# Kernel tuning notes

Measured on AMD Instinct MI355X. Metric: run time of the kernel, lower is better.

The kernel has to match this reference:

```python
import jax, jax.numpy as jnp
import numpy as np

N_NODES = 100000
N_EDGES = 1600000
IN_C, HID_C, OUT_C = 128, 128, 64


def setup_inputs() -> dict:
    key = jax.random.key(0)
    ks = jax.random.split(key, 6)
    x = jax.random.normal(ks[0], (N_NODES, IN_C), dtype=jnp.float32)
    edge_index = jax.random.randint(ks[1], (2, N_EDGES), 0, N_NODES)
    W1 = jax.random.normal(ks[2], (IN_C, HID_C), dtype=jnp.float32) * (1.0 / np.sqrt(IN_C))
    b1 = jnp.zeros((HID_C,), dtype=jnp.float32)
    W2 = jax.random.normal(ks[3], (HID_C, OUT_C), dtype=jnp.float32) * (1.0 / np.sqrt(HID_C))
    b2 = jnp.zeros((OUT_C,), dtype=jnp.float32)
    return {"x": x, "edge_index": edge_index, "W1": W1, "b1": b1, "W2": W2, "b2": b2}


def gcn_conv(x, W, b, src, dst):
    # PyG GCNConv: D^{-1/2} (A + I) D^{-1/2} X W + b, with self-loops handled
    # analytically (no explicit self-loop edges materialized).
    h = x @ W                                             # [N, d_out]
    ones = jnp.ones(src.shape[0], dtype=h.dtype)
    deg = jax.ops.segment_sum(ones, dst, num_segments=N_NODES) + 1.0  # +1 self-loop
    dinv = jax.lax.rsqrt(deg)                             # deg >= 1, safe
    norm = dinv[src] * dinv[dst]                          # [E]
    msg = h[src] * norm[:, None]                          # gather + scale  [E, d_out]
    agg = jax.ops.segment_sum(msg, dst, num_segments=N_NODES)
    agg = agg + h * (dinv * dinv)[:, None]                # self-loop contribution
    return agg + b


def reference(x, edge_index, W1, b1, W2, b2):
    src, dst = edge_index[0], edge_index[1]
    h = jax.nn.relu(gcn_conv(x, W1, b1, src, dst))
    # dropout is identity in eval mode
    out = gcn_conv(h, W2, b2, src, dst)
    return out
```

## Files before the change

### kernel.cpp

```cpp
#include <hip/hip_runtime.h>

#define N_NODESC 100000
#define N_EDGESC 1600000
#define NB_BUCKETS 391
#define BUCKET_CAP 5120
#define CHUNK_A 4096

typedef __attribute__((ext_vector_type(4))) float floatx4;
typedef __attribute__((ext_vector_type(8))) short shortx8;

__device__ __forceinline__ unsigned short f32_to_bf16_rne(float f) {
    unsigned int u = __float_as_uint(f);
    unsigned int r = u + 0x7fffu + ((u >> 16) & 1u);
    return (unsigned short)(r >> 16);
}
__device__ __forceinline__ float bf16_to_f32(unsigned short h) {
    return __uint_as_float(((unsigned int)h) << 16);
}
__device__ __forceinline__ float bflo(unsigned int u) { return __uint_as_float(u << 16); }
__device__ __forceinline__ float bfhi(unsigned int u) { return __uint_as_float(u & 0xffff0000u); }
__device__ __forceinline__ unsigned int pack2bf(float a, float b) {
    return ((unsigned int)f32_to_bf16_rne(b) << 16) | (unsigned int)f32_to_bf16_rne(a);
}

__global__ __launch_bounds__(256) void k_wfrag_all(const float* __restrict__ W1,
        const float* __restrict__ W2,
        unsigned short* __restrict__ w1hi, unsigned short* __restrict__ w1lo,
        unsigned short* __restrict__ w2hi, unsigned short* __restrict__ w2lo,
        int* __restrict__ gcur) {
    int t = threadIdx.x;
    if (blockIdx.x == 0)
        for (int i = t; i < NB_BUCKETS; i += 256) gcur[i] = i * BUCKET_CAP;
    int idx = blockIdx.x * 256 + t;
    float f;
    int k, col, C, o;
    unsigned short *phi, *plo;
    if (idx < 16384) {
        k = idx >> 7; col = idx & 127; C = 8;
        f = W1[idx]; phi = w1hi; plo = w1lo;
    } else {
        int idx2 = idx - 16384;
        k = idx2 >> 6; col = idx2 & 63; C = 4;
        f = W2[idx2]; phi = w2hi; plo = w2lo;
    }
    unsigned short hi = f32_to_bf16_rne(f);
    unsigned short lo = f32_to_bf16_rne(f - bf16_to_f32(hi));
    int kc = k >> 5, q = (k >> 3) & 3, j = k & 7;
    int c = col >> 4, n = col & 15;
    o = (((kc * C + c) * 4 + q) * 16 + n) * 8 + j;
    phi[o] = hi; plo[o] = lo;
}

__global__ __launch_bounds__(1024) void k_bucket(const int* __restrict__ src,
        const int* __restrict__ dst, int* __restrict__ gcur,
        unsigned int* __restrict__ tmp) {
    __shared__ int hist[NB_BUCKETS];
    int t = threadIdx.x;
    for (int i = t; i < NB_BUCKETS; i += 1024) hist[i] = 0;
    __syncthreads();
    int base = blockIdx.x * CHUNK_A;
    int end = min(base + CHUNK_A, N_EDGESC);
    for (int e = base + t; e < end; e += 1024)
        atomicAdd(&hist[dst[e] >> 8], 1);
    __syncthreads();
    for (int i = t; i < NB_BUCKETS; i += 1024) {
        int c = hist[i];
        hist[i] = (c > 0) ? atomicAdd(&gcur[i], c) : 0;
    }
    __syncthreads();
    for (int e = base + t; e < end; e += 1024) {
        int d = dst[e];
        int pos = atomicAdd(&hist[d >> 8], 1);
        tmp[pos] = ((unsigned int)src[e] << 8) | (unsigned int)(d & 255);
    }
}

__global__ __launch_bounds__(1024) void k_place(const unsigned int* __restrict__ tmp,
        const int* __restrict__ gcur,
        int* __restrict__ swsrc, int* __restrict__ deg,
        int* __restrict__ row_ptr, float* __restrict__ dinv) {
    __shared__ int hist[256], scan[256], lcur[256];
    int b = blockIdx.x, t = threadIdx.x;
    int start = b * BUCKET_CAP;
    int end = gcur[b];
    if (t < 256) hist[t] = 0;
    __syncthreads();
    for (int i = start + t; i < end; i += 1024)
        atomicAdd(&hist[tmp[i] & 255u], 1);
    __syncthreads();
    int own = (t < 256) ? hist[t] : 0;
    if (t < 256) scan[t] = own;
    __syncthreads();
    for (int off = 1; off < 256; off <<= 1) {
        int add = (t >= off && t < 256) ? scan[t - off] : 0;
        __syncthreads();
        if (t < 256) scan[t] += add;
        __syncthreads();
    }
    if (t < 256) {
        int rp = start + scan[t] - own;
        lcur[t] = rp;
        int node = (b << 8) + t;
        if (node < N_NODESC) {
            deg[node] = own;
            row_ptr[node] = rp;
            dinv[node] = rsqrtf((float)own + 1.0f);
        }
    }
    __syncthreads();
    for (int i = start + t; i < end; i += 1024) {
        unsigned int v = tmp[i];
        int pos = atomicAdd(&lcur[v & 255u], 1);
        swsrc[pos] = (int)(v >> 8);
    }
}

template<int NOUT, int AFP32>
__global__ __launch_bounds__(256) void k_gemm_mfma(const void* __restrict__ Xv,
        const unsigned short* __restrict__ whi, const unsigned short* __restrict__ wlo,
        const float* __restrict__ dinv, unsigned short* __restrict__ H) {
    constexpr int C = NOUT / 16;
    constexpr int PITCH = NOUT + 4;
    __shared__ __align__(16) float etile[4][16][PITCH];
    int wv = threadIdx.x >> 6, lane = threadIdx.x & 63;
    int n16 = lane & 15, q = lane >> 4;
    int rowBase = blockIdx.x * 128 + wv * 32;
    floatx4 acc[2][C];
#pragma unroll
    for (int m = 0; m < 2; ++m)
#pragma unroll
        for (int c = 0; c < C; ++c) acc[m][c] = (floatx4){0.f, 0.f, 0.f, 0.f};

    const shortx8* whi8 = (const shortx8*)whi;
    const shortx8* wlo8 = (const shortx8*)wlo;

    for (int kc = 0; kc < 4; ++kc) {
        shortx8 ahi[2], alo[2];
#pragma unroll
        for (int m = 0; m < 2; ++m) {
            int r = rowBase + m * 16 + n16;
            if (r >= N_NODESC) r = N_NODESC - 1;
            if (AFP32) {
                const float* xp = &((const float*)Xv)[(size_t)r * 128 + kc * 32 + q * 8];
                floatx4 x0 = *(const floatx4*)xp;
                floatx4 x1 = *(const floatx4*)(xp + 4);
#pragma unroll
                for (int jj = 0; jj < 4; ++jj) {
                    unsigned short h0 = f32_to_bf16_rne(x0[jj]);
                    ahi[m][jj] = (short)h0;
                    alo[m][jj] = (short)f32_to_bf16_rne(x0[jj] - bf16_to_f32(h0));
                    unsigned short h1 = f32_to_bf16_rne(x1[jj]);
                    ahi[m][jj + 4] = (short)h1;
                    alo[m][jj + 4] = (short)f32_to_bf16_rne(x1[jj] - bf16_to_f32(h1));
                }
            } else {
                const unsigned short* xp = &((const unsigned short*)Xv)[(size_t)r * 128 + kc * 32 + q * 8];
                ahi[m] = *(const shortx8*)xp;
            }
        }
#pragma unroll
        for (int c = 0; c < C; ++c) {
            int fo = (kc * C + c) * 64 + lane;
            shortx8 bhi = whi8[fo];
            shortx8 blo = wlo8[fo];
#pragma unroll
            for (int m = 0; m < 2; ++m) {
                acc[m][c] = __builtin_amdgcn_mfma_f32_16x16x32_bf16(ahi[m], bhi, acc[m][c], 0, 0, 0);
                if (AFP32)
                    acc[m][c] = __builtin_amdgcn_mfma_f32_16x16x32_bf16(alo[m], bhi, acc[m][c], 0, 0, 0);
                acc[m][c] = __builtin_amdgcn_mfma_f32_16x16x32_bf16(ahi[m], blo, acc[m][c], 0, 0, 0);
            }
        }
    }
    constexpr int CPL = NOUT / 4;
#pragma unroll
    for (int m = 0; m < 2; ++m) {
        __builtin_amdgcn_wave_barrier();
#pragma unroll
        for (int c = 0; c < C; ++c)
#pragma unroll
            for (int reg = 0; reg < 4; ++reg)
                etile[wv][q * 4 + reg][c * 16 + n16] = acc[m][c][reg];
        asm volatile("s_waitcnt lgkmcnt(0)" ::: "memory");
        __builtin_amdgcn_wave_barrier();
        int row = lane >> 2, cb = lane & 3;
        int r = rowBase + m * 16 + row;
        if (r < N_NODESC) {
            float dv = dinv[r];
            unsigned int po[CPL / 2];
#pragma unroll
            for (int i = 0; i < CPL / 4; ++i) {
                floatx4 v = *(const floatx4*)&etile[wv][row][cb * CPL + i * 4];
                po[i * 2 + 0] = pack2bf(v[0] * dv, v[1] * dv);
                po[i * 2 + 1] = pack2bf(v[2] * dv, v[3] * dv);
            }
            unsigned int* op = (unsigned int*)&H[(size_t)r * NOUT + cb * CPL];
#pragma unroll
            for (int i = 0; i < CPL / 8; ++i)
                *(uint4*)(op + i * 4) = *(uint4*)&po[i * 4];
        }
        asm volatile("s_waitcnt lgkmcnt(0)" ::: "memory");
        __builtin_amdgcn_wave_barrier();
    }
}

__global__ __launch_bounds__(256) void k_agg_gemm(const unsigned short* __restrict__ Hb,
        const int* __restrict__ swsrc, const int* __restrict__ row_ptr,
        const int* __restrict__ deg, const float* __restrict__ dinv,
        const float* __restrict__ bias,
        const unsigned short* __restrict__ w2hi, const unsigned short* __restrict__ w2lo,
        unsigned short* __restrict__ H2) {
    __shared__ __align__(16) unsigned int lds_h[16][64];
    int wv = threadIdx.x >> 6, lane = threadIdx.x & 63;
    int g = lane >> 4, l16 = lane & 15;
    int nb = blockIdx.x * 16;

#pragma unroll
    for (int i = 0; i < 4; ++i) {
        int nt = wv * 4 + i;
        int node = nb + nt;
        int start = row_ptr[node];
        int end = start + deg[node];
        float acc[8] = {0.f, 0.f, 0.f, 0.f, 0.f, 0.f, 0.f, 0.f};
        int j = start + g;
        for (; j + 4 < end; j += 8) {
            int s0 = swsrc[j];
            int s1 = swsrc[j + 4];
            uint4 v0 = *(const uint4*)(Hb + (size_t)s0 * 128 + l16 * 8);
            uint4 v1 = *(const uint4*)(Hb + (size_t)s1 * 128 + l16 * 8);
            acc[0] += bflo(v0.x) + bflo(v1.x);
            acc[1] += bfhi(v0.x) + bfhi(v1.x);
            acc[2] += bflo(v0.y) + bflo(v1.y);
            acc[3] += bfhi(v0.y) + bfhi(v1.y);
            acc[4] += bflo(v0.z) + bflo(v1.z);
            acc[5] += bfhi(v0.z) + bfhi(v1.z);
            acc[6] += bflo(v0.w) + bflo(v1.w);
            acc[7] += bfhi(v0.w) + bfhi(v1.w);
        }
        if (j < end) {
            int s0 = swsrc[j];
            uint4 v0 = *(const uint4*)(Hb + (size_t)s0 * 128 + l16 * 8);
            acc[0] += bflo(v0.x); acc[1] += bfhi(v0.x);
            acc[2] += bflo(v0.y); acc[3] += bfhi(v0.y);
            acc[4] += bflo(v0.z); acc[5] += bfhi(v0.z);
            acc[6] += bflo(v0.w); acc[7] += bfhi(v0.w);
        }
#pragma unroll
        for (int k = 0; k < 8; ++k) {
            acc[k] += __shfl_xor(acc[k], 16);
            acc[k] += __shfl_xor(acc[k], 32);
        }
        if (g == 0) {
            float dv = dinv[node];
            uint4 sv = *(const uint4*)(Hb + (size_t)node * 128 + l16 * 8);
            floatx4 b0 = *(const floatx4*)&bias[l16 * 8];
            floatx4 b1 = *(const floatx4*)&bias[l16 * 8 + 4];
            float o0 = dv * (acc[0] + bflo(sv.x)) + b0[0];
            float o1 = dv * (acc[1] + bfhi(sv.x)) + b0[1];
            float o2 = dv * (acc[2] + bflo(sv.y)) + b0[2];
            float o3 = dv * (acc[3] + bfhi(sv.y)) + b0[3];
            float o4 = dv * (acc[4] + bflo(sv.z)) + b1[0];
            float o5 = dv * (acc[5] + bfhi(sv.z)) + b1[1];
            float o6 = dv * (acc[6] + bflo(sv.w)) + b1[2];
            float o7 = dv * (acc[7] + bfhi(sv.w)) + b1[3];
            uint4 o;
            o.x = pack2bf(fmaxf(o0, 0.f), fmaxf(o1, 0.f));
            o.y = pack2bf(fmaxf(o2, 0.f), fmaxf(o3, 0.f));
            o.z = pack2bf(fmaxf(o4, 0.f), fmaxf(o5, 0.f));
            o.w = pack2bf(fmaxf(o6, 0.f), fmaxf(o7, 0.f));
            int pcol = (l16 * 4) ^ ((nt & 7) * 4);
            *(uint4*)&lds_h[nt][pcol] = o;
        }
    }
    __syncthreads();

    int q = lane >> 4, n16 = lane & 15;
    floatx4 accm = (floatx4){0.f, 0.f, 0.f, 0.f};
    const shortx8* whi8 = (const shortx8*)w2hi;
    const shortx8* wlo8 = (const shortx8*)w2lo;
#pragma unroll
    for (int kc = 0; kc < 4; ++kc) {
        int pcol = (kc * 16 + q * 4) ^ ((n16 & 7) * 4);
        shortx8 ahi = *(const shortx8*)&lds_h[n16][pcol];
        int fo = (kc * 4 + wv) * 64 + lane;
        shortx8 bhi = whi8[fo];
        shortx8 blo = wlo8[fo];
        accm = __builtin_amdgcn_mfma_f32_16x16x32_bf16(ahi, bhi, accm, 0, 0, 0);
        accm = __builtin_amdgcn_mfma_f32_16x16x32_bf16(ahi, blo, accm, 0, 0, 0);
    }
    int crow = (lane >> 4) * 4;
    int ccol = wv * 16 + n16;
#pragma unroll
    for (int reg = 0; reg < 4; ++reg) {
        int r = nb + crow + reg;
        float dv = dinv[r];
        H2[(size_t)r * 64 + ccol] = f32_to_bf16_rne(accm[reg] * dv);
    }
}

__global__ __launch_bounds__(256) void k_agg64(const unsigned short* __restrict__ Hb,
        const int* __restrict__ swsrc, const int* __restrict__ row_ptr,
        const int* __restrict__ deg, const float* __restrict__ dinv,
        const float* __restrict__ bias, float* __restrict__ out) {
    int node = blockIdx.x * 4 + (threadIdx.x >> 6);
    int lane = threadIdx.x & 63;
    int g = lane >> 3, l8 = lane & 7;
    int start = row_ptr[node];
    int end = start + deg[node];
    float acc[8] = {0.f, 0.f, 0.f, 0.f, 0.f, 0.f, 0.f, 0.f};
    int j = start + g;
    for (; j + 8 < end; j += 16) {
        int s0 = swsrc[j];
        int s1 = swsrc[j + 8];
        uint4 v0 = *(const uint4*)(Hb + (size_t)s0 * 64 + l8 * 8);
        uint4 v1 = *(const uint4*)(Hb + (size_t)s1 * 64 + l8 * 8);
        acc[0] += bflo(v0.x) + bflo(v1.x);
        acc[1] += bfhi(v0.x) + bfhi(v1.x);
        acc[2] += bflo(v0.y) + bflo(v1.y);
        acc[3] += bfhi(v0.y) + bfhi(v1.y);
        acc[4] += bflo(v0.z) + bflo(v1.z);
        acc[5] += bfhi(v0.z) + bfhi(v1.z);
        acc[6] += bflo(v0.w) + bflo(v1.w);
        acc[7] += bfhi(v0.w) + bfhi(v1.w);
    }
    if (j < end) {
        int s0 = swsrc[j];
        uint4 v0 = *(const uint4*)(Hb + (size_t)s0 * 64 + l8 * 8);
        acc[0] += bflo(v0.x); acc[1] += bfhi(v0.x);
        acc[2] += bflo(v0.y); acc[3] += bfhi(v0.y);
        acc[4] += bflo(v0.z); acc[5] += bfhi(v0.z);
        acc[6] += bflo(v0.w); acc[7] += bfhi(v0.w);
    }
#pragma unroll
    for (int i = 0; i < 8; ++i) {
        acc[i] += __shfl_xor(acc[i], 8);
        acc[i] += __shfl_xor(acc[i], 16);
        acc[i] += __shfl_xor(acc[i], 32);
    }
    if (g == 0) {
        float dv = dinv[node];
        uint4 sv = *(const uint4*)(Hb + (size_t)node * 64 + l8 * 8);
        floatx4 b0 = *(const floatx4*)&bias[l8 * 8];
        floatx4 b1 = *(const floatx4*)&bias[l8 * 8 + 4];
        floatx4 o0, o1;
        o0[0] = dv * (acc[0] + bflo(sv.x)) + b0[0];
        o0[1] = dv * (acc[1] + bfhi(sv.x)) + b0[1];
        o0[2] = dv * (acc[2] + bflo(sv.y)) + b0[2];
        o0[3] = dv * (acc[3] + bfhi(sv.y)) + b0[3];
        o1[0] = dv * (acc[4] + bflo(sv.z)) + b1[0];
        o1[1] = dv * (acc[5] + bfhi(sv.z)) + b1[1];
        o1[2] = dv * (acc[6] + bflo(sv.w)) + b1[2];
        o1[3] = dv * (acc[7] + bfhi(sv.w)) + b1[3];
        *(floatx4*)&out[(size_t)node * 64 + l8 * 8] = o0;
        *(floatx4*)&out[(size_t)node * 64 + l8 * 8 + 4] = o1;
    }
}

extern "C" void kernel_launch(void* const* d_in, const int* in_sizes, int n_in,
                              void* d_out, int out_size, void* d_ws, size_t ws_size,
                              hipStream_t stream) {
    const float* x  = (const float*)d_in[0];
    const int*   ei = (const int*)d_in[1];
    const float* W1 = (const float*)d_in[2];
    const float* b1 = (const float*)d_in[3];
    const float* W2 = (const float*)d_in[4];
    const float* b2 = (const float*)d_in[5];
    float* out = (float*)d_out;
    const int* src = ei;
    const int* dst = ei + N_EDGESC;

    char* ws = (char*)d_ws;
    size_t off = 0;
    auto alloc = [&](size_t bytes) -> void* {
        off = (off + 255) & ~(size_t)255;
        void* p = ws + off;
        off += bytes;
        return p;
    };
    const size_t CSR_SLOTS = (size_t)NB_BUCKETS * BUCKET_CAP;
    int*   deg     = (int*)  alloc((size_t)N_NODESC * 4);
    float* dinv    = (float*)alloc((size_t)N_NODESC * 4);
    int*   row_ptr = (int*)  alloc((size_t)N_NODESC * 4);
    int*   gcur    = (int*)  alloc(NB_BUCKETS * 4);
    unsigned int* tmp   = (unsigned int*)alloc(CSR_SLOTS * 4);
    int*   swsrc   = (int*)  alloc(CSR_SLOTS * 4);
    unsigned short* w1hi = (unsigned short*)alloc(128 * 128 * 2);
    unsigned short* w1lo = (unsigned short*)alloc(128 * 128 * 2);
    unsigned short* w2hi = (unsigned short*)alloc(128 * 64 * 2);
    unsigned short* w2lo = (unsigned short*)alloc(128 * 64 * 2);
    unsigned short* h1b  = (unsigned short*)alloc((size_t)N_NODESC * 128 * 2);
    unsigned short* h2b  = (unsigned short*)alloc((size_t)N_NODESC * 128 * 2);

    const int nbGemm = (N_NODESC + 127) / 128;
    const int nbBkt  = (N_EDGESC + CHUNK_A - 1) / CHUNK_A;

    k_wfrag_all<<<(16384 + 8192) / 256, 256, 0, stream>>>(W1, W2, w1hi, w1lo, w2hi, w2lo, gcur);
    k_bucket<<<nbBkt, 1024, 0, stream>>>(src, dst, gcur, tmp);
    k_place<<<NB_BUCKETS, 1024, 0, stream>>>(tmp, gcur, swsrc, deg, row_ptr, dinv);

    k_gemm_mfma<128, 1><<<nbGemm, 256, 0, stream>>>(x, w1hi, w1lo, dinv, h1b);
    k_agg_gemm<<<N_NODESC / 16, 256, 0, stream>>>(h1b, swsrc, row_ptr, deg, dinv, b1,
                                                  w2hi, w2lo, h2b);
    k_agg64<<<N_NODESC / 4, 256, 0, stream>>>(h2b, swsrc, row_ptr, deg, dinv, b2, out);
}
```

Before: 278.0 us.

## Make aggregate-GEMM wave-independent via register shuffles and stage buckets in LDS

The fused aggregation+GEMM kernel now gives each wave 16 whole nodes and builds the MFMA A-fragments in registers through cross-lane shuffles. This removes the shared LDS tile and the block-wide barrier, and each wave computes all four output column blocks itself. The cost is more shuffles and redundant weight loads per wave. Separately, k_place copies each bucket into LDS once, so the histogram and placement passes no longer read the global tmp array twice.

```diff
diff --git a/kernel.cpp b/kernel.cpp
--- a/kernel.cpp
+++ b/kernel.cpp
@@ -79,14 +79,16 @@
         const int* __restrict__ gcur,
         int* __restrict__ swsrc, int* __restrict__ deg,
         int* __restrict__ row_ptr, float* __restrict__ dinv) {
+    __shared__ unsigned int eb[BUCKET_CAP];
     __shared__ int hist[256], scan[256], lcur[256];
     int b = blockIdx.x, t = threadIdx.x;
     int start = b * BUCKET_CAP;
-    int end = gcur[b];
+    int cnt = gcur[b] - start;
     if (t < 256) hist[t] = 0;
-    __syncthreads();
-    for (int i = start + t; i < end; i += 1024)
-        atomicAdd(&hist[tmp[i] & 255u], 1);
+    for (int i = t; i < cnt; i += 1024) eb[i] = tmp[start + i];
+    __syncthreads();
+    for (int i = t; i < cnt; i += 1024)
+        atomicAdd(&hist[eb[i] & 255u], 1);
     __syncthreads();
     int own = (t < 256) ? hist[t] : 0;
     if (t < 256) scan[t] = own;
@@ -108,8 +110,8 @@
         }
     }
     __syncthreads();
-    for (int i = start + t; i < end; i += 1024) {
-        unsigned int v = tmp[i];
+    for (int i = t; i < cnt; i += 1024) {
+        unsigned int v = eb[i];
         int pos = atomicAdd(&lcur[v & 255u], 1);
         swsrc[pos] = (int)(v >> 8);
     }
@@ -210,91 +212,118 @@
         const float* __restrict__ bias,
         const unsigned short* __restrict__ w2hi, const unsigned short* __restrict__ w2lo,
         unsigned short* __restrict__ H2) {
-    __shared__ __align__(16) unsigned int lds_h[16][64];
     int wv = threadIdx.x >> 6, lane = threadIdx.x & 63;
     int g = lane >> 4, l16 = lane & 15;
-    int nb = blockIdx.x * 16;
-
-#pragma unroll
-    for (int i = 0; i < 4; ++i) {
-        int nt = wv * 4 + i;
-        int node = nb + nt;
-        int start = row_ptr[node];
-        int end = start + deg[node];
-        float acc[8] = {0.f, 0.f, 0.f, 0.f, 0.f, 0.f, 0.f, 0.f};
-        int j = start + g;
-        for (; j + 4 < end; j += 8) {
-            int s0 = swsrc[j];
-            int s1 = swsrc[j + 4];
-            uint4 v0 = *(const uint4*)(Hb + (size_t)s0 * 128 + l16 * 8);
-            uint4 v1 = *(const uint4*)(Hb + (size_t)s1 * 128 + l16 * 8);
-            acc[0] += bflo(v0.x) + bflo(v1.x);
-            acc[1] += bfhi(v0.x) + bfhi(v1.x);
-            acc[2] += bflo(v0.y) + bflo(v1.y);
-            acc[3] += bfhi(v0.y) + bfhi(v1.y);
-            acc[4] += bflo(v0.z) + bflo(v1.z);
-            acc[5] += bfhi(v0.z) + bfhi(v1.z);
-            acc[6] += bflo(v0.w) + bflo(v1.w);
-            acc[7] += bfhi(v0.w) + bfhi(v1.w);
-        }
-        if (j < end) {
-            int s0 = swsrc[j];
-            uint4 v0 = *(const uint4*)(Hb + (size_t)s0 * 128 + l16 * 8);
-            acc[0] += bflo(v0.x); acc[1] += bfhi(v0.x);
-            acc[2] += bflo(v0.y); acc[3] += bfhi(v0.y);
-            acc[4] += bflo(v0.z); acc[5] += bfhi(v0.z);
-            acc[6] += bflo(v0.w); acc[7] += bfhi(v0.w);
-        }
-#pragma unroll
-        for (int k = 0; k < 8; ++k) {
-            acc[k] += __shfl_xor(acc[k], 16);
-            acc[k] += __shfl_xor(acc[k], 32);
-        }
-        if (g == 0) {
+    int nb = blockIdx.x * 64 + wv * 16;
+
+    unsigned int frag[4][4];
+#pragma unroll
+    for (int kc = 0; kc < 4; ++kc)
+#pragma unroll
+        for (int w = 0; w < 4; ++w) frag[kc][w] = 0u;
+
+    floatx4 b0 = *(const floatx4*)&bias[l16 * 8];
+    floatx4 b1 = *(const floatx4*)&bias[l16 * 8 + 4];
+
+    for (int i = 0; i < 16; ++i) {
+        int node = nb + i;
+        unsigned int o0 = 0, o1 = 0, o2 = 0, o3 = 0;
+        if (node < N_NODESC) {
+            int start = row_ptr[node];
+            int end = start + deg[node];
+            float acc[8] = {0.f, 0.f, 0.f, 0.f, 0.f, 0.f, 0.f, 0.f};
+            int j = start + g;
+            for (; j + 4 < end; j += 8) {
+                int s0 = swsrc[j];
+                int s1 = swsrc[j + 4];
+                uint4 v0 = *(const uint4*)(Hb + (size_t)s0 * 128 + l16 * 8);
+                uint4 v1 = *(const uint4*)(Hb + (size_t)s1 * 128 + l16 * 8);
+                acc[0] += bflo(v0.x) + bflo(v1.x);
+                acc[1] += bfhi(v0.x) + bfhi(v1.x);
+                acc[2] += bflo(v0.y) + bflo(v1.y);
+                acc[3] += bfhi(v0.y) + bfhi(v1.y);
+                acc[4] += bflo(v0.z) + bflo(v1.z);
+                acc[5] += bfhi(v0.z) + bfhi(v1.z);
+                acc[6] += bflo(v0.w) + bflo(v1.w);
+                acc[7] += bfhi(v0.w) + bfhi(v1.w);
+            }
+            if (j < end) {
+                int s0 = swsrc[j];
+                uint4 v0 = *(const uint4*)(Hb + (size_t)s0 * 128 + l16 * 8);
+                acc[0] += bflo(v0.x); acc[1] += bfhi(v0.x);
+                acc[2] += bflo(v0.y); acc[3] += bfhi(v0.y);
+                acc[4] += bflo(v0.z); acc[5] += bfhi(v0.z);
+                acc[6] += bflo(v0.w); acc[7] += bfhi(v0.w);
+            }
+#pragma unroll
+            for (int k = 0; k < 8; ++k) {
+                acc[k] += __shfl_xor(acc[k], 16);
+                acc[k] += __shfl_xor(acc[k], 32);
+            }
             float dv = dinv[node];
             uint4 sv = *(const uint4*)(Hb + (size_t)node * 128 + l16 * 8);
-            floatx4 b0 = *(const floatx4*)&bias[l16 * 8];
-            floatx4 b1 = *(const floatx4*)&bias[l16 * 8 + 4];
-            float o0 = dv * (acc[0] + bflo(sv.x)) + b0[0];
-            float o1 = dv * (acc[1] + bfhi(sv.x)) + b0[1];
-            float o2 = dv * (acc[2] + bflo(sv.y)) + b0[2];
-            float o3 = dv * (acc[3] + bfhi(sv.y)) + b0[3];
-            float o4 = dv * (acc[4] + bflo(sv.z)) + b1[0];
-            float o5 = dv * (acc[5] + bfhi(sv.z)) + b1[1];
-            float o6 = dv * (acc[6] + bflo(sv.w)) + b1[2];
-            float o7 = dv * (acc[7] + bfhi(sv.w)) + b1[3];
-            uint4 o;
-            o.x = pack2bf(fmaxf(o0, 0.f), fmaxf(o1, 0.f));
-            o.y = pack2bf(fmaxf(o2, 0.f), fmaxf(o3, 0.f));
-            o.z = pack2bf(fmaxf(o4, 0.f), fmaxf(o5, 0.f));
-            o.w = pack2bf(fmaxf(o6, 0.f), fmaxf(o7, 0.f));
-            int pcol = (l16 * 4) ^ ((nt & 7) * 4);
-            *(uint4*)&lds_h[nt][pcol] = o;
-        }
-    }
-    __syncthreads();
-
-    int q = lane >> 4, n16 = lane & 15;
-    floatx4 accm = (floatx4){0.f, 0.f, 0.f, 0.f};
+            float e0 = dv * (acc[0] + bflo(sv.x)) + b0[0];
+            float e1 = dv * (acc[1] + bfhi(sv.x)) + b0[1];
+            float e2 = dv * (acc[2] + bflo(sv.y)) + b0[2];
+            float e3 = dv * (acc[3] + bfhi(sv.y)) + b0[3];
+            float e4 = dv * (acc[4] + bflo(sv.z)) + b1[0];
+            float e5 = dv * (acc[5] + bfhi(sv.z)) + b1[1];
+            float e6 = dv * (acc[6] + bflo(sv.w)) + b1[2];
+            float e7 = dv * (acc[7] + bfhi(sv.w)) + b1[3];
+            o0 = pack2bf(fmaxf(e0, 0.f), fmaxf(e1, 0.f));
+            o1 = pack2bf(fmaxf(e2, 0.f), fmaxf(e3, 0.f));
+            o2 = pack2bf(fmaxf(e4, 0.f), fmaxf(e5, 0.f));
+            o3 = pack2bf(fmaxf(e6, 0.f), fmaxf(e7, 0.f));
+        }
+        bool mine = (l16 == i);
+#pragma unroll
+        for (int kc = 0; kc < 4; ++kc) {
+            int srcl = kc * 4 + (lane >> 4);
+            unsigned int w0 = __shfl(o0, srcl);
+            unsigned int w1 = __shfl(o1, srcl);
+            unsigned int w2 = __shfl(o2, srcl);
+            unsigned int w3 = __shfl(o3, srcl);
+            if (mine) {
+                frag[kc][0] = w0; frag[kc][1] = w1;
+                frag[kc][2] = w2; frag[kc][3] = w3;
+            }
+        }
+    }
+
+    shortx8 a[4];
+#pragma unroll
+    for (int kc = 0; kc < 4; ++kc)
+#pragma unroll
+        for (int w = 0; w < 4; ++w)
+            ((unsigned int*)&a[kc])[w] = frag[kc][w];
+
     const shortx8* whi8 = (const shortx8*)w2hi;
     const shortx8* wlo8 = (const shortx8*)w2lo;
-#pragma unroll
-    for (int kc = 0; kc < 4; ++kc) {
-        int pcol = (kc * 16 + q * 4) ^ ((n16 & 7) * 4);
-        shortx8 ahi = *(const shortx8*)&lds_h[n16][pcol];
-        int fo = (kc * 4 + wv) * 64 + lane;
-        shortx8 bhi = whi8[fo];
-        shortx8 blo = wlo8[fo];
-        accm = __builtin_amdgcn_mfma_f32_16x16x32_bf16(ahi, bhi, accm, 0, 0, 0);
-        accm = __builtin_amdgcn_mfma_f32_16x16x32_bf16(ahi, blo, accm, 0, 0, 0);
-    }
     int crow = (lane >> 4) * 4;
-    int ccol = wv * 16 + n16;
+    float dv4[4];
 #pragma unroll
     for (int reg = 0; reg < 4; ++reg) {
         int r = nb + crow + reg;
-        float dv = dinv[r];
-        H2[(size_t)r * 64 + ccol] = f32_to_bf16_rne(accm[reg] * dv);
+        dv4[reg] = (r < N_NODESC) ? dinv[r] : 0.f;
+    }
+#pragma unroll
+    for (int cb = 0; cb < 4; ++cb) {
+        floatx4 accm = (floatx4){0.f, 0.f, 0.f, 0.f};
+#pragma unroll
+        for (int kc = 0; kc < 4; ++kc) {
+            int fo = (kc * 4 + cb) * 64 + lane;
+            shortx8 bhi = whi8[fo];
+            shortx8 blo = wlo8[fo];
+            accm = __builtin_amdgcn_mfma_f32_16x16x32_bf16(a[kc], bhi, accm, 0, 0, 0);
+            accm = __builtin_amdgcn_mfma_f32_16x16x32_bf16(a[kc], blo, accm, 0, 0, 0);
+        }
+        int ccol = cb * 16 + (lane & 15);
+#pragma unroll
+        for (int reg = 0; reg < 4; ++reg) {
+            int r = nb + crow + reg;
+            if (r < N_NODESC)
+                H2[(size_t)r * 64 + ccol] = f32_to_bf16_rne(accm[reg] * dv4[reg]);
+        }
     }
 }
 
@@ -393,13 +422,14 @@
 
     const int nbGemm = (N_NODESC + 127) / 128;
     const int nbBkt  = (N_EDGESC + CHUNK_A - 1) / CHUNK_A;
+    const int nbAgg  = (N_NODESC + 63) / 64;
 
     k_wfrag_all<<<(16384 + 8192) / 256, 256, 0, stream>>>(W1, W2, w1hi, w1lo, w2hi, w2lo, gcur);
     k_bucket<<<nbBkt, 1024, 0, stream>>>(src, dst, gcur, tmp);
     k_place<<<NB_BUCKETS, 1024, 0, stream>>>(tmp, gcur, swsrc, deg, row_ptr, dinv);
 
     k_gemm_mfma<128, 1><<<nbGemm, 256, 0, stream>>>(x, w1hi, w1lo, dinv, h1b);
-    k_agg_gemm<<<N_NODESC / 16, 256, 0, stream>>>(h1b, swsrc, row_ptr, deg, dinv, b1,
-                                                  w2hi, w2lo, h2b);
+    k_agg_gemm<<<nbAgg, 256, 0, stream>>>(h1b, swsrc, row_ptr, deg, dinv, b1,
+                                          w2hi, w2lo, h2b);
     k_agg64<<<N_NODESC / 4, 256, 0, stream>>>(h2b, swsrc, row_ptr, deg, dinv, b2, out);
 }
```

New measurement: 313.2 us. +12.7%, slower.

## Fuse edge bucketing with first GEMM and move source-side dinv into aggregation

Applied to the files above, without the earlier changes.

The edge-bucketing pass and the layer-1 X·W1 GEMM now share one launch, with the first blocks doing bucketing and the rest doing the GEMM. This works because the GEMM no longer scales rows by dinv; the dinv[src] factor is applied per edge in the aggregation, so the GEMM no longer waits on degree computation. k_place also stages each bucket in shared memory so tmp is read from global memory only once. The cost is an extra dinv gather per edge in layer-1 aggregation, plus a different block size and chunk size for bucketing.

```diff
diff --git a/kernel.cpp b/kernel.cpp
--- a/kernel.cpp
+++ b/kernel.cpp
@@ -4,7 +4,8 @@
 #define N_EDGESC 1600000
 #define NB_BUCKETS 391
 #define BUCKET_CAP 5120
-#define CHUNK_A 4096
+#define CHUNK_A 2048
+#define NBKT_BLOCKS ((N_EDGESC + CHUNK_A - 1) / CHUNK_A)
 
 typedef __attribute__((ext_vector_type(4))) float floatx4;
 typedef __attribute__((ext_vector_type(8))) short shortx8;
@@ -51,27 +52,105 @@
     phi[o] = hi; plo[o] = lo;
 }
 
-__global__ __launch_bounds__(1024) void k_bucket(const int* __restrict__ src,
-        const int* __restrict__ dst, int* __restrict__ gcur,
-        unsigned int* __restrict__ tmp) {
-    __shared__ int hist[NB_BUCKETS];
-    int t = threadIdx.x;
-    for (int i = t; i < NB_BUCKETS; i += 1024) hist[i] = 0;
-    __syncthreads();
-    int base = blockIdx.x * CHUNK_A;
-    int end = min(base + CHUNK_A, N_EDGESC);
-    for (int e = base + t; e < end; e += 1024)
-        atomicAdd(&hist[dst[e] >> 8], 1);
-    __syncthreads();
-    for (int i = t; i < NB_BUCKETS; i += 1024) {
-        int c = hist[i];
-        hist[i] = (c > 0) ? atomicAdd(&gcur[i], c) : 0;
-    }
-    __syncthreads();
-    for (int e = base + t; e < end; e += 1024) {
-        int d = dst[e];
-        int pos = atomicAdd(&hist[d >> 8], 1);
-        tmp[pos] = ((unsigned int)src[e] << 8) | (unsigned int)(d & 255);
+__global__ __launch_bounds__(256) void k_fusedA(const float* __restrict__ x,
+        const unsigned short* __restrict__ w1hi, const unsigned short* __restrict__ w1lo,
+        const int* __restrict__ src, const int* __restrict__ dst,
+        int* __restrict__ gcur, unsigned int* __restrict__ tmp,
+        unsigned short* __restrict__ H) {
+    __shared__ __align__(16) float etile[4][16][132];
+    if (blockIdx.x < NBKT_BLOCKS) {
+        int* hist = (int*)etile;
+        int t = threadIdx.x;
+        for (int i = t; i < NB_BUCKETS; i += 256) hist[i] = 0;
+        __syncthreads();
+        int base = blockIdx.x * CHUNK_A;
+        int end = min(base + CHUNK_A, N_EDGESC);
+        for (int e = base + t; e < end; e += 256)
+            atomicAdd(&hist[dst[e] >> 8], 1);
+        __syncthreads();
+        for (int i = t; i < NB_BUCKETS; i += 256) {
+            int c = hist[i];
+            hist[i] = (c > 0) ? atomicAdd(&gcur[i], c) : 0;
+        }
+        __syncthreads();
+        for (int e = base + t; e < end; e += 256) {
+            int d = dst[e];
+            int pos = atomicAdd(&hist[d >> 8], 1);
+            tmp[pos] = ((unsigned int)src[e] << 8) | (unsigned int)(d & 255);
+        }
+        return;
+    }
+    int wv = threadIdx.x >> 6, lane = threadIdx.x & 63;
+    int n16 = lane & 15, q = lane >> 4;
+    int rowBase = (blockIdx.x - NBKT_BLOCKS) * 128 + wv * 32;
+    floatx4 acc[2][8];
+#pragma unroll
+    for (int m = 0; m < 2; ++m)
+#pragma unroll
+        for (int c = 0; c < 8; ++c) acc[m][c] = (floatx4){0.f, 0.f, 0.f, 0.f};
+
+    const shortx8* whi8 = (const shortx8*)w1hi;
+    const shortx8* wlo8 = (const shortx8*)w1lo;
+
+    for (int kc = 0; kc < 4; ++kc) {
+        shortx8 ahi[2], alo[2];
+#pragma unroll
+        for (int m = 0; m < 2; ++m) {
+            int r = rowBase + m * 16 + n16;
+            if (r >= N_NODESC) r = N_NODESC - 1;
+            const float* xp = &x[(size_t)r * 128 + kc * 32 + q * 8];
+            floatx4 x0 = *(const floatx4*)xp;
+            floatx4 x1 = *(const floatx4*)(xp + 4);
+#pragma unroll
+            for (int jj = 0; jj < 4; ++jj) {
+                unsigned short h0 = f32_to_bf16_rne(x0[jj]);
+                ahi[m][jj] = (short)h0;
+                alo[m][jj] = (short)f32_to_bf16_rne(x0[jj] - bf16_to_f32(h0));
+                unsigned short h1 = f32_to_bf16_rne(x1[jj]);
+                ahi[m][jj + 4] = (short)h1;
+                alo[m][jj + 4] = (short)f32_to_bf16_rne(x1[jj] - bf16_to_f32(h1));
+            }
+        }
+#pragma unroll
+        for (int c = 0; c < 8; ++c) {
+            int fo = (kc * 8 + c) * 64 + lane;
+            shortx8 bhi = whi8[fo];
+            shortx8 blo = wlo8[fo];
+#pragma unroll
+            for (int m = 0; m < 2; ++m) {
+                acc[m][c] = __builtin_amdgcn_mfma_f32_16x16x32_bf16(ahi[m], bhi, acc[m][c], 0, 0, 0);
+                acc[m][c] = __builtin_amdgcn_mfma_f32_16x16x32_bf16(alo[m], bhi, acc[m][c], 0, 0, 0);
+                acc[m][c] = __builtin_amdgcn_mfma_f32_16x16x32_bf16(ahi[m], blo, acc[m][c], 0, 0, 0);
+            }
+        }
+    }
+#pragma unroll
+    for (int m = 0; m < 2; ++m) {
+        __builtin_amdgcn_wave_barrier();
+#pragma unroll
+        for (int c = 0; c < 8; ++c)
+#pragma unroll
+            for (int reg = 0; reg < 4; ++reg)
+                etile[wv][q * 4 + reg][c * 16 + n16] = acc[m][c][reg];
+        asm volatile("s_waitcnt lgkmcnt(0)" ::: "memory");
+        __builtin_amdgcn_wave_barrier();
+        int row = lane >> 2, cb = lane & 3;
+        int r = rowBase + m * 16 + row;
+        if (r < N_NODESC) {
+            unsigned int po[16];
+#pragma unroll
+            for (int i = 0; i < 8; ++i) {
+                floatx4 v = *(const floatx4*)&etile[wv][row][cb * 32 + i * 4];
+                po[i * 2 + 0] = pack2bf(v[0], v[1]);
+                po[i * 2 + 1] = pack2bf(v[2], v[3]);
+            }
+            unsigned int* op = (unsigned int*)&H[(size_t)r * 128 + cb * 32];
+#pragma unroll
+            for (int i = 0; i < 4; ++i)
+                *(uint4*)(op + i * 4) = *(uint4*)&po[i * 4];
+        }
+        asm volatile("s_waitcnt lgkmcnt(0)" ::: "memory");
+        __builtin_amdgcn_wave_barrier();
     }
 }
 
@@ -79,14 +158,16 @@
         const int* __restrict__ gcur,
         int* __restrict__ swsrc, int* __restrict__ deg,
         int* __restrict__ row_ptr, float* __restrict__ dinv) {
+    __shared__ unsigned int eb[BUCKET_CAP];
     __shared__ int hist[256], scan[256], lcur[256];
     int b = blockIdx.x, t = threadIdx.x;
     int start = b * BUCKET_CAP;
-    int end = gcur[b];
+    int cnt = gcur[b] - start;
     if (t < 256) hist[t] = 0;
-    __syncthreads();
-    for (int i = start + t; i < end; i += 1024)
-        atomicAdd(&hist[tmp[i] & 255u], 1);
+    for (int i = t; i < cnt; i += 1024) eb[i] = tmp[start + i];
+    __syncthreads();
+    for (int i = t; i < cnt; i += 1024)
+        atomicAdd(&hist[eb[i] & 255u], 1);
     __syncthreads();
     int own = (t < 256) ? hist[t] : 0;
     if (t < 256) scan[t] = own;
@@ -108,99 +189,10 @@
         }
     }
     __syncthreads();
-    for (int i = start + t; i < end; i += 1024) {
-        unsigned int v = tmp[i];
+    for (int i = t; i < cnt; i += 1024) {
+        unsigned int v = eb[i];
         int pos = atomicAdd(&lcur[v & 255u], 1);
         swsrc[pos] = (int)(v >> 8);
-    }
-}
-
-template<int NOUT, int AFP32>
-__global__ __launch_bounds__(256) void k_gemm_mfma(const void* __restrict__ Xv,
-        const unsigned short* __restrict__ whi, const unsigned short* __restrict__ wlo,
-        const float* __restrict__ dinv, unsigned short* __restrict__ H) {
-    constexpr int C = NOUT / 16;
-    constexpr int PITCH = NOUT + 4;
-    __shared__ __align__(16) float etile[4][16][PITCH];
-    int wv = threadIdx.x >> 6, lane = threadIdx.x & 63;
-    int n16 = lane & 15, q = lane >> 4;
-    int rowBase = blockIdx.x * 128 + wv * 32;
-    floatx4 acc[2][C];
-#pragma unroll
-    for (int m = 0; m < 2; ++m)
-#pragma unroll
-        for (int c = 0; c < C; ++c) acc[m][c] = (floatx4){0.f, 0.f, 0.f, 0.f};
-
-    const shortx8* whi8 = (const shortx8*)whi;
-    const shortx8* wlo8 = (const shortx8*)wlo;
-
-    for (int kc = 0; kc < 4; ++kc) {
-        shortx8 ahi[2], alo[2];
-#pragma unroll
-        for (int m = 0; m < 2; ++m) {
-            int r = rowBase + m * 16 + n16;
-            if (r >= N_NODESC) r = N_NODESC - 1;
-            if (AFP32) {
-                const float* xp = &((const float*)Xv)[(size_t)r * 128 + kc * 32 + q * 8];
-                floatx4 x0 = *(const floatx4*)xp;
-                floatx4 x1 = *(const floatx4*)(xp + 4);
-#pragma unroll
-                for (int jj = 0; jj < 4; ++jj) {
-                    unsigned short h0 = f32_to_bf16_rne(x0[jj]);
-                    ahi[m][jj] = (short)h0;
-                    alo[m][jj] = (short)f32_to_bf16_rne(x0[jj] - bf16_to_f32(h0));
-                    unsigned short h1 = f32_to_bf16_rne(x1[jj]);
-                    ahi[m][jj + 4] = (short)h1;
-                    alo[m][jj + 4] = (short)f32_to_bf16_rne(x1[jj] - bf16_to_f32(h1));
-                }
-            } else {
-                const unsigned short* xp = &((const unsigned short*)Xv)[(size_t)r * 128 + kc * 32 + q * 8];
-                ahi[m] = *(const shortx8*)xp;
-            }
-        }
-#pragma unroll
-        for (int c = 0; c < C; ++c) {
-            int fo = (kc * C + c) * 64 + lane;
-            shortx8 bhi = whi8[fo];
-            shortx8 blo = wlo8[fo];
-#pragma unroll
-            for (int m = 0; m < 2; ++m) {
-                acc[m][c] = __builtin_amdgcn_mfma_f32_16x16x32_bf16(ahi[m], bhi, acc[m][c], 0, 0, 0);
-                if (AFP32)
-                    acc[m][c] = __builtin_amdgcn_mfma_f32_16x16x32_bf16(alo[m], bhi, acc[m][c], 0, 0, 0);
-                acc[m][c] = __builtin_amdgcn_mfma_f32_16x16x32_bf16(ahi[m], blo, acc[m][c], 0, 0, 0);
-            }
-        }
-    }
-    constexpr int CPL = NOUT / 4;
-#pragma unroll
-    for (int m = 0; m < 2; ++m) {
-        __builtin_amdgcn_wave_barrier();
-#pragma unroll
-        for (int c = 0; c < C; ++c)
-#pragma unroll
-            for (int reg = 0; reg < 4; ++reg)
-                etile[wv][q * 4 + reg][c * 16 + n16] = acc[m][c][reg];
-        asm volatile("s_waitcnt lgkmcnt(0)" ::: "memory");
-        __builtin_amdgcn_wave_barrier();
-        int row = lane >> 2, cb = lane & 3;
-        int r = rowBase + m * 16 + row;
-        if (r < N_NODESC) {
-            float dv = dinv[r];
-            unsigned int po[CPL / 2];
-#pragma unroll
-            for (int i = 0; i < CPL / 4; ++i) {
-                floatx4 v = *(const floatx4*)&etile[wv][row][cb * CPL + i * 4];
-                po[i * 2 + 0] = pack2bf(v[0] * dv, v[1] * dv);
-                po[i * 2 + 1] = pack2bf(v[2] * dv, v[3] * dv);
-            }
-            unsigned int* op = (unsigned int*)&H[(size_t)r * NOUT + cb * CPL];
-#pragma unroll
-            for (int i = 0; i < CPL / 8; ++i)
-                *(uint4*)(op + i * 4) = *(uint4*)&po[i * 4];
-        }
-        asm volatile("s_waitcnt lgkmcnt(0)" ::: "memory");
-        __builtin_amdgcn_wave_barrier();
     }
 }
 
@@ -226,24 +218,27 @@
         for (; j + 4 < end; j += 8) {
             int s0 = swsrc[j];
             int s1 = swsrc[j + 4];
+            float dv0 = dinv[s0];
+            float dv1 = dinv[s1];
             uint4 v0 = *(const uint4*)(Hb + (size_t)s0 * 128 + l16 * 8);
             uint4 v1 = *(const uint4*)(Hb + (size_t)s1 * 128 + l16 * 8);
-            acc[0] += bflo(v0.x) + bflo(v1.x);
-            acc[1] += bfhi(v0.x) + bfhi(v1.x);
-            acc[2] += bflo(v0.y) + bflo(v1.y);
-            acc[3] += bfhi(v0.y) + bfhi(v1.y);
-            acc[4] += bflo(v0.z) + bflo(v1.z);
-            acc[5] += bfhi(v0.z) + bfhi(v1.z);
-            acc[6] += bflo(v0.w) + bflo(v1.w);
-            acc[7] += bfhi(v0.w) + bfhi(v1.w);
+            acc[0] += dv0 * bflo(v0.x) + dv1 * bflo(v1.x);
+            acc[1] += dv0 * bfhi(v0.x) + dv1 * bfhi(v1.x);
+            acc[2] += dv0 * bflo(v0.y) + dv1 * bflo(v1.y);
+            acc[3] += dv0 * bfhi(v0.y) + dv1 * bfhi(v1.y);
+            acc[4] += dv0 * bflo(v0.z) + dv1 * bflo(v1.z);
+            acc[5] += dv0 * bfhi(v0.z) + dv1 * bfhi(v1.z);
+            acc[6] += dv0 * bflo(v0.w) + dv1 * bflo(v1.w);
+            acc[7] += dv0 * bfhi(v0.w) + dv1 * bfhi(v1.w);
         }
         if (j < end) {
             int s0 = swsrc[j];
+            float dv0 = dinv[s0];
             uint4 v0 = *(const uint4*)(Hb + (size_t)s0 * 128 + l16 * 8);
-            acc[0] += bflo(v0.x); acc[1] += bfhi(v0.x);
-            acc[2] += bflo(v0.y); acc[3] += bfhi(v0.y);
-            acc[4] += bflo(v0.z); acc[5] += bfhi(v0.z);
-            acc[6] += bflo(v0.w); acc[7] += bfhi(v0.w);
+            acc[0] += dv0 * bflo(v0.x); acc[1] += dv0 * bfhi(v0.x);
+            acc[2] += dv0 * bflo(v0.y); acc[3] += dv0 * bfhi(v0.y);
+            acc[4] += dv0 * bflo(v0.z); acc[5] += dv0 * bfhi(v0.z);
+            acc[6] += dv0 * bflo(v0.w); acc[7] += dv0 * bfhi(v0.w);
         }
 #pragma unroll
         for (int k = 0; k < 8; ++k) {
@@ -255,19 +250,19 @@
             uint4 sv = *(const uint4*)(Hb + (size_t)node * 128 + l16 * 8);
             floatx4 b0 = *(const floatx4*)&bias[l16 * 8];
             floatx4 b1 = *(const floatx4*)&bias[l16 * 8 + 4];
-            float o0 = dv * (acc[0] + bflo(sv.x)) + b0[0];
-            float o1 = dv * (acc[1] + bfhi(sv.x)) + b0[1];
-            float o2 = dv * (acc[2] + bflo(sv.y)) + b0[2];
-            float o3 = dv * (acc[3] + bfhi(sv.y)) + b0[3];
-            float o4 = dv * (acc[4] + bflo(sv.z)) + b1[0];
-            float o5 = dv * (acc[5] + bfhi(sv.z)) + b1[1];
-            float o6 = dv * (acc[6] + bflo(sv.w)) + b1[2];
-            float o7 = dv * (acc[7] + bfhi(sv.w)) + b1[3];
+            float e0 = dv * (acc[0] + dv * bflo(sv.x)) + b0[0];
+            float e1 = dv * (acc[1] + dv * bfhi(sv.x)) + b0[1];
+            float e2 = dv * (acc[2] + dv * bflo(sv.y)) + b0[2];
+            float e3 = dv * (acc[3] + dv * bfhi(sv.y)) + b0[3];
+            float e4 = dv * (acc[4] + dv * bflo(sv.z)) + b1[0];
+            float e5 = dv * (acc[5] + dv * bfhi(sv.z)) + b1[1];
+            float e6 = dv * (acc[6] + dv * bflo(sv.w)) + b1[2];
+            float e7 = dv * (acc[7] + dv * bfhi(sv.w)) + b1[3];
             uint4 o;
-            o.x = pack2bf(fmaxf(o0, 0.f), fmaxf(o1, 0.f));
-            o.y = pack2bf(fmaxf(o2, 0.f), fmaxf(o3, 0.f));
-            o.z = pack2bf(fmaxf(o4, 0.f), fmaxf(o5, 0.f));
-            o.w = pack2bf(fmaxf(o6, 0.f), fmaxf(o7, 0.f));
+            o.x = pack2bf(fmaxf(e0, 0.f), fmaxf(e1, 0.f));
+            o.y = pack2bf(fmaxf(e2, 0.f), fmaxf(e3, 0.f));
+            o.z = pack2bf(fmaxf(e4, 0.f), fmaxf(e5, 0.f));
+            o.w = pack2bf(fmaxf(e6, 0.f), fmaxf(e7, 0.f));
             int pcol = (l16 * 4) ^ ((nt & 7) * 4);
             *(uint4*)&lds_h[nt][pcol] = o;
         }
@@ -392,13 +387,12 @@
     unsigned short* h2b  = (unsigned short*)alloc((size_t)N_NODESC * 128 * 2);
 
     const int nbGemm = (N_NODESC + 127) / 128;
-    const int nbBkt  = (N_EDGESC + CHUNK_A - 1) / CHUNK_A;
 
     k_wfrag_all<<<(16384 + 8192) / 256, 256, 0, stream>>>(W1, W2, w1hi, w1lo, w2hi, w2lo, gcur);
-    k_bucket<<<nbBkt, 1024, 0, stream>>>(src, dst, gcur, tmp);
+    k_fusedA<<<NBKT_BLOCKS + nbGemm, 256, 0, stream>>>(x, w1hi, w1lo, src, dst,
+                                                       gcur, tmp, h1b);
     k_place<<<NB_BUCKETS, 1024, 0, stream>>>(tmp, gcur, swsrc, deg, row_ptr, dinv);
 
-    k_gemm_mfma<128, 1><<<nbGemm, 256, 0, stream>>>(x, w1hi, w1lo, dinv, h1b);
     k_agg_gemm<<<N_NODESC / 16, 256, 0, stream>>>(h1b, swsrc, row_ptr, deg, dinv, b1,
                                                   w2hi, w2lo, h2b);
     k_agg64<<<N_NODESC / 4, 256, 0, stream>>>(h2b, swsrc, row_ptr, deg, dinv, b2, out);
```

Result: slower. 289.0 us (+4.0%).
